# Kernel tuning notes

Measured on AMD Instinct MI355X. Metric: run time of the kernel, lower is better.

The kernel has to match this reference:

```python
import jax, jax.numpy as jnp
import numpy as np

N, E, IN, HID, H, C = 10000, 320000, 64, 64, 4, 64
HC = H * C  # 256


def setup_inputs() -> dict:
    key = jax.random.key(0)
    ks = jax.random.split(key, 40)
    ki = iter(range(40))
    def nrm(shape, scale=0.05):
        return jax.random.normal(ks[next(ki)], shape, dtype=jnp.float32) * scale
    inp = {
        "x": jax.random.normal(ks[next(ki)], (N, IN), dtype=jnp.float32),
        "edge_index": jax.random.randint(ks[next(ki)], (2, E), 0, N, dtype=jnp.int64),
        "lin_w": nrm((IN, HID)), "lin_b": nrm((HID,)),
    }
    dims_in = [HID, HC, HC]
    for i, di in enumerate(dims_in):
        inp[f"gat_w{i}"] = nrm((di, HC))
        inp[f"att_src{i}"] = nrm((H, C))
        inp[f"att_dst{i}"] = nrm((H, C))
        inp[f"gat_b{i}"] = nrm((HC,))
        inp[f"ln_g{i}"] = jnp.ones((HC,), jnp.float32)
        inp[f"ln_b{i}"] = jnp.zeros((HC,), jnp.float32)
    inp["ffn_w1"] = nrm((HC, 2 * HID)); inp["ffn_b1"] = nrm((2 * HID,))
    inp["ffn_w2"] = nrm((2 * HID, 64)); inp["ffn_b2"] = nrm((64,))
    return inp


def _layernorm(x, g, b, eps=1e-5):
    m = jnp.mean(x, -1, keepdims=True)
    v = jnp.var(x, -1, keepdims=True)
    return (x - m) * jax.lax.rsqrt(v + eps) * g + b


def _gat(x, src, dst, w, a_src, a_dst, b):
    # PyG GATConv: per-head linear, additive attention, segment softmax over dst
    xl = (x @ w).reshape(-1, H, C)              # [N,H,C]
    e = jax.nn.leaky_relu(jnp.sum(xl * a_src, -1)[src]
                          + jnp.sum(xl * a_dst, -1)[dst], 0.2)  # [E,H]
    emax = jax.ops.segment_max(e, dst, num_segments=N)
    ex = jnp.exp(e - emax[dst])
    alpha = ex / jax.ops.segment_sum(ex, dst, num_segments=N)[dst]
    out = jax.ops.segment_sum(xl[src] * alpha[:, :, None], dst, num_segments=N)
    return out.reshape(-1, HC) + b


def reference(x, edge_index, lin_w, lin_b,
              gat_w0, att_src0, att_dst0, gat_b0, ln_g0, ln_b0,
              gat_w1, att_src1, att_dst1, gat_b1, ln_g1, ln_b1,
              gat_w2, att_src2, att_dst2, gat_b2, ln_g2, ln_b2,
              ffn_w1, ffn_b1, ffn_w2, ffn_b2):
    loops = jnp.arange(N, dtype=edge_index.dtype)
    src = jnp.concatenate([edge_index[0], loops])  # add_self_loops=True
    dst = jnp.concatenate([edge_index[1], loops])
    h = jax.nn.relu(x @ lin_w + lin_b)
    layers = [(gat_w0, att_src0, att_dst0, gat_b0, ln_g0, ln_b0),
              (gat_w1, att_src1, att_dst1, gat_b1, ln_g1, ln_b1),
              (gat_w2, att_src2, att_dst2, gat_b2, ln_g2, ln_b2)]
    for (w, a_s, a_d, b, g, lb) in layers:
        residual = h
        h = jax.nn.elu(_gat(h, src, dst, w, a_s, a_d, b))
        if residual.shape[-1] != h.shape[-1]:
            residual = jnp.pad(residual, ((0, 0), (0, h.shape[-1] - residual.shape[-1])))
        h = _layernorm(h + residual, g, lb)  # dropout is identity in eval mode
    h = jax.nn.relu(h @ ffn_w1 + ffn_b1)
    return h @ ffn_w2 + ffn_b2
```

## Files before the change

### kernel.cpp

```cpp
#include <hip/hip_runtime.h>

#define N_NODES 10000
#define N_EDGES 320000
#define EL (N_EDGES + N_NODES)
#define HC 256
#define CAP 96

using bf16x8 = __attribute__((ext_vector_type(8))) short;
using f32x4  = __attribute__((ext_vector_type(4))) float;

__device__ __forceinline__ float bf2f(unsigned short u) {
  union { unsigned int i; float f; } v; v.i = ((unsigned int)u) << 16; return v.f;
}
__device__ __forceinline__ unsigned short f2bf(float f) {
  union { float f; unsigned int i; } v; v.f = f;
  unsigned int r = (v.i + 0x7FFFu + ((v.i >> 16) & 1u)) >> 16;
  return (unsigned short)r;
}


__global__ __launch_bounds__(256) void prep_kernel(int* __restrict__ cnt) {
  int i = blockIdx.x * 256 + threadIdx.x;
  if (i < N_NODES) cnt[i] = 0;
}


__device__ __forceinline__ void convw_body(const float* __restrict__ w,
                                           unsigned short* __restrict__ bt,
                                           int K, int idx) {
  int half = K >> 1;
  int col = idx / half;
  int k2 = (idx % half) * 2;
  ushort2 o;
  o.x = f2bf(w[(size_t)k2 * 256 + col]);
  o.y = f2bf(w[(size_t)(k2 + 1) * 256 + col]);
  *(ushort2*)(bt + (size_t)col * K + k2) = o;
}

__global__ __launch_bounds__(256) void scatter_lin_kernel(
    const int* __restrict__ edges, int* __restrict__ cnt, int* __restrict__ slots,
    const float* __restrict__ A, const float* __restrict__ B,
    const float* __restrict__ bias, unsigned short* __restrict__ C,
    const float* __restrict__ w0, unsigned short* __restrict__ bt0,
    const float* __restrict__ w1, unsigned short* __restrict__ bt1,
    const float* __restrict__ w2, unsigned short* __restrict__ bt2) {
  int tid = threadIdx.x;
  int b = blockIdx.x;
  if (b < 1290) {
    int e = b * 256 + tid;
    if (e >= EL) return;
    int s, d;
    if (e < N_EDGES) { s = edges[e]; d = edges[N_EDGES + e]; }
    else { s = d = e - N_EDGES; }
    int pos = atomicAdd(&cnt[d], 1);
    slots[d * CAP + pos] = s;
    return;
  }
  if (b >= 1915) {
    if (b < 1947) convw_body(w0, bt0, 64, (b - 1915) * 256 + tid);
    else if (b < 2075) convw_body(w1, bt1, 256, (b - 1947) * 256 + tid);
    else convw_body(w2, bt2, 256, (b - 2075) * 256 + tid);
    return;
  }
  __shared__ float As[16][36];
  __shared__ float Bs[32][64];
  int row0 = (b - 1290) * 16;
  int g = tid >> 6, lane = tid & 63;
  float acc[4] = {0.f, 0.f, 0.f, 0.f};
  for (int k0 = 0; k0 < 64; k0 += 32) {
    if (tid < 128) {
      int r = tid >> 3;
      int kc = (tid & 7) << 2;
      *(float4*)&As[r][kc] = *(const float4*)(A + (size_t)(row0 + r) * 64 + k0 + kc);
    }
#pragma unroll
    for (int i = 0; i < 2; ++i) {
      int fidx = (i * 256 + tid) * 4;
      *(float4*)&Bs[fidx >> 6][fidx & 63] =
          *(const float4*)(B + (size_t)(k0 + (fidx >> 6)) * 64 + (fidx & 63));
    }
    __syncthreads();
#pragma unroll
    for (int kk = 0; kk < 32; kk += 4) {
      float a4[4][4];
#pragma unroll
      for (int rr = 0; rr < 4; ++rr) {
        float4 t = *(const float4*)&As[g * 4 + rr][kk];
        a4[rr][0] = t.x; a4[rr][1] = t.y; a4[rr][2] = t.z; a4[rr][3] = t.w;
      }
#pragma unroll
      for (int u = 0; u < 4; ++u) {
        float bb = Bs[kk + u][lane];
#pragma unroll
        for (int rr = 0; rr < 4; ++rr) acc[rr] = fmaf(a4[rr][u], bb, acc[rr]);
      }
    }
    __syncthreads();
  }
#pragma unroll
  for (int rr = 0; rr < 4; ++rr) {
    int row = row0 + g * 4 + rr;
    C[(size_t)row * 64 + lane] = f2bf(fmaxf(acc[rr] + bias[lane], 0.f));
  }
}


template <int K>
__global__ __launch_bounds__(256) void gemm_attn_mfma(
    const unsigned short* __restrict__ A, const unsigned short* __restrict__ Bt,
    unsigned short* __restrict__ Cb,
    const float* __restrict__ att_src, const float* __restrict__ att_dst,
    float* __restrict__ asrc_out, float* __restrict__ adst_out) {
  __shared__ __align__(16) unsigned short Asw[16 * 64];
  __shared__ __align__(16) unsigned short Bsw[256 * 64];
  int tid = threadIdx.x;
  int wave = tid >> 6, lane = tid & 63;
  int r = lane & 15, g = lane >> 4;
  int row0 = blockIdx.x * 16;

  f32x4 acc[4];
#pragma unroll
  for (int i = 0; i < 4; ++i) acc[i] = {0.f, 0.f, 0.f, 0.f};

  for (int k0 = 0; k0 < K; k0 += 64) {
    {
      int ar = tid >> 4;
      int kc = (tid & 15) << 2;
      ushort4 av = *(const ushort4*)(A + (size_t)(row0 + ar) * K + k0 + kc);
      *(ushort4*)((char*)Asw + ((ar * 128 + kc * 2) ^ ((ar & 7) << 4))) = av;
    }
#pragma unroll
    for (int i = 0; i < 8; ++i) {
      int idx = i * 256 + tid;
      int col = idx >> 3;
      int kc8 = idx & 7;
      uint4 v = *(const uint4*)(Bt + (size_t)col * K + k0 + kc8 * 8);
      *(uint4*)((char*)Bsw + ((col * 128 + kc8 * 16) ^ ((col & 7) << 4))) = v;
    }
    __syncthreads();
#pragma unroll
    for (int chunk = 0; chunk < 2; ++chunk) {
      bf16x8 af = *(const bf16x8*)((char*)Asw +
                    ((r * 128 + chunk * 64 + g * 16) ^ ((r & 7) << 4)));
#pragma unroll
      for (int i = 0; i < 4; ++i) {
        int col = (wave * 4 + i) * 16 + r;
        bf16x8 bfr = *(const bf16x8*)((char*)Bsw +
                       ((col * 128 + chunk * 64 + g * 16) ^ ((col & 7) << 4)));
        acc[i] = __builtin_amdgcn_mfma_f32_16x16x32_bf16(af, bfr, acc[i], 0, 0, 0);
      }
    }
    __syncthreads();
  }

  float asv[4], adv[4];
#pragma unroll
  for (int i = 0; i < 4; ++i) {
    int col = (wave * 4 + i) * 16 + r;
    asv[i] = att_src[col];
    adv[i] = att_dst[col];
  }
#pragma unroll
  for (int j = 0; j < 4; ++j) {
    float ps = acc[0][j] * asv[0] + acc[1][j] * asv[1] + acc[2][j] * asv[2] + acc[3][j] * asv[3];
    float pd = acc[0][j] * adv[0] + acc[1][j] * adv[1] + acc[2][j] * adv[2] + acc[3][j] * adv[3];
#pragma unroll
    for (int m = 8; m >= 1; m >>= 1) {
      ps += __shfl_xor(ps, m);
      pd += __shfl_xor(pd, m);
    }
    if (r == 0) {
      int row = row0 + g * 4 + j;
      asrc_out[row * 4 + wave] = ps;
      adst_out[row * 4 + wave] = pd;
    }
  }

#pragma unroll
  for (int i = 0; i < 4; ++i) {
    int col = (wave * 4 + i) * 16 + r;
#pragma unroll
    for (int j = 0; j < 4; ++j) {
      int row = row0 + g * 4 + j;
      Cb[(size_t)row * 256 + col] = f2bf(acc[i][j]);
    }
  }
}


template <int MODE>
__global__ __launch_bounds__(256) void agg_kernel(
    const int* __restrict__ cnt, const int* __restrict__ slots,
    const float* __restrict__ asrc, const float* __restrict__ adst,
    const unsigned short* __restrict__ xb, const float* __restrict__ bias,
    const unsigned short* __restrict__ resid, const float* __restrict__ ln_g,
    const float* __restrict__ ln_b, unsigned short* __restrict__ hout) {
  int w = threadIdx.x >> 6, lane = threadIdx.x & 63;
  int n = blockIdx.x * 4 + w;
  int lh = lane & 31;
  int half = lane >> 5;
  int h = lh >> 3;
  int ch8 = lh << 3;
  float ad = adst[n * 4 + h];

  int i0 = n * CAP;
  int deg = cnt[n];
  int len0 = (deg + 1) >> 1;
  int beg = i0 + (half ? len0 : 0);
  int end = i0 + (half ? deg : len0);
  int last = end - 1;

  float a0 = 0.f, a1 = 0.f, a2 = 0.f, a3 = 0.f, a4 = 0.f, a5 = 0.f, a6 = 0.f, a7 = 0.f;
  float wsum = 0.f;

  int sA[4];
#pragma unroll
  for (int j = 0; j < 4; ++j) sA[j] = slots[min(beg + j, last)];
  float ca[4]; uint4 cx[4];
#pragma unroll
  for (int j = 0; j < 4; ++j) {
    ca[j] = asrc[sA[j] * 4 + h];
    cx[j] = *(const uint4*)(xb + (size_t)sA[j] * HC + ch8);
  }
#pragma unroll
  for (int j = 0; j < 4; ++j) sA[j] = slots[min(beg + 4 + j, last)];

  for (int base = beg; base < end; base += 4) {
    float na[4]; uint4 nx[4];
#pragma unroll
    for (int j = 0; j < 4; ++j) {
      na[j] = asrc[sA[j] * 4 + h];
      nx[j] = *(const uint4*)(xb + (size_t)sA[j] * HC + ch8);
    }
#pragma unroll
    for (int j = 0; j < 4; ++j) sA[j] = slots[min(base + 8 + j, last)];
#pragma unroll
    for (int j = 0; j < 4; ++j) {
      float e = ca[j] + ad;
      e = e > 0.f ? e : 0.2f * e;
      float wg = __expf(e);
      wg = (base + j < end) ? wg : 0.f;
      wsum += wg;
      a0 = fmaf(wg, bf2f((unsigned short)(cx[j].x & 0xffff)), a0);
      a1 = fmaf(wg, bf2f((unsigned short)(cx[j].x >> 16)), a1);
      a2 = fmaf(wg, bf2f((unsigned short)(cx[j].y & 0xffff)), a2);
      a3 = fmaf(wg, bf2f((unsigned short)(cx[j].y >> 16)), a3);
      a4 = fmaf(wg, bf2f((unsigned short)(cx[j].z & 0xffff)), a4);
      a5 = fmaf(wg, bf2f((unsigned short)(cx[j].z >> 16)), a5);
      a6 = fmaf(wg, bf2f((unsigned short)(cx[j].w & 0xffff)), a6);
      a7 = fmaf(wg, bf2f((unsigned short)(cx[j].w >> 16)), a7);
    }
#pragma unroll
    for (int j = 0; j < 4; ++j) { ca[j] = na[j]; cx[j] = nx[j]; }
  }

  a0 += __shfl_xor(a0, 32); a1 += __shfl_xor(a1, 32);
  a2 += __shfl_xor(a2, 32); a3 += __shfl_xor(a3, 32);
  a4 += __shfl_xor(a4, 32); a5 += __shfl_xor(a5, 32);
  a6 += __shfl_xor(a6, 32); a7 += __shfl_xor(a7, 32);
  wsum += __shfl_xor(wsum, 32);

  int cb = ch8 + half * 4;
  float v0 = half ? a4 : a0;
  float v1 = half ? a5 : a1;
  float v2 = half ? a6 : a2;
  float v3 = half ? a7 : a3;

  float rw = 1.f / wsum;
  float4 b4 = *(const float4*)(bias + cb);
  v0 = fmaf(v0, rw, b4.x);
  v1 = fmaf(v1, rw, b4.y);
  v2 = fmaf(v2, rw, b4.z);
  v3 = fmaf(v3, rw, b4.w);
  v0 = v0 > 0.f ? v0 : __expf(v0) - 1.f;
  v1 = v1 > 0.f ? v1 : __expf(v1) - 1.f;
  v2 = v2 > 0.f ? v2 : __expf(v2) - 1.f;
  v3 = v3 > 0.f ? v3 : __expf(v3) - 1.f;

  if constexpr (MODE == 0) {
    if (cb < 64) {
      ushort4 r4 = *(const ushort4*)(resid + (size_t)n * 64 + cb);
      v0 += bf2f(r4.x); v1 += bf2f(r4.y); v2 += bf2f(r4.z); v3 += bf2f(r4.w);
    }
  } else {
    ushort4 r4 = *(const ushort4*)(resid + (size_t)n * HC + cb);
    v0 += bf2f(r4.x); v1 += bf2f(r4.y); v2 += bf2f(r4.z); v3 += bf2f(r4.w);
  }

  float s1 = v0 + v1 + v2 + v3;
  float s2 = v0 * v0 + v1 * v1 + v2 * v2 + v3 * v3;
#pragma unroll
  for (int m = 32; m >= 1; m >>= 1) {
    s1 += __shfl_xor(s1, m);
    s2 += __shfl_xor(s2, m);
  }
  float mean = s1 * (1.f / 256.f);
  float var = s2 * (1.f / 256.f) - mean * mean;
  float inv = rsqrtf(var + 1e-5f);

  float4 g4 = *(const float4*)(ln_g + cb);
  float4 lb4 = *(const float4*)(ln_b + cb);
  ushort4 o;
  o.x = f2bf((v0 - mean) * inv * g4.x + lb4.x);
  o.y = f2bf((v1 - mean) * inv * g4.y + lb4.y);
  o.z = f2bf((v2 - mean) * inv * g4.z + lb4.z);
  o.w = f2bf((v3 - mean) * inv * g4.w + lb4.w);
  *(ushort4*)(hout + (size_t)n * HC + cb) = o;
}


__global__ __launch_bounds__(256) void ffn_kernel(const unsigned short* __restrict__ A,
                                                  const float* __restrict__ w1,
                                                  const float* __restrict__ b1,
                                                  const float* __restrict__ w2,
                                                  const float* __restrict__ b2,
                                                  float* __restrict__ out) {
  __shared__ float As[16][36];
  __shared__ float Bs[32][128];
  __shared__ float Ms[16][132];
  int tid = threadIdx.x;
  int row0 = blockIdx.x * 16;
  int g = tid >> 6, lane = tid & 63;

  {
    int colBase = lane * 2;
    float acc[4][2];
#pragma unroll
    for (int r = 0; r < 4; ++r) { acc[r][0] = 0.f; acc[r][1] = 0.f; }
    for (int k0 = 0; k0 < 256; k0 += 32) {
      if (tid < 128) {
        int r = tid >> 3;
        int kc = (tid & 7) << 2;
        ushort4 av = *(const ushort4*)(A + (size_t)(row0 + r) * 256 + k0 + kc);
        As[r][kc]     = bf2f(av.x);
        As[r][kc + 1] = bf2f(av.y);
        As[r][kc + 2] = bf2f(av.z);
        As[r][kc + 3] = bf2f(av.w);
      }
#pragma unroll
      for (int i = 0; i < 4; ++i) {
        int fidx = (i * 256 + tid) * 4;
        *(float4*)&Bs[fidx >> 7][fidx & 127] =
            *(const float4*)(w1 + (size_t)(k0 + (fidx >> 7)) * 128 + (fidx & 127));
      }
      __syncthreads();
#pragma unroll
      for (int kk = 0; kk < 32; kk += 4) {
        float a4[4][4];
#pragma unroll
        for (int rr = 0; rr < 4; ++rr) {
          float4 tv = *(const float4*)&As[g * 4 + rr][kk];
          a4[rr][0] = tv.x; a4[rr][1] = tv.y; a4[rr][2] = tv.z; a4[rr][3] = tv.w;
        }
#pragma unroll
        for (int u = 0; u < 4; ++u) {
          float2 b = *(const float2*)&Bs[kk + u][colBase];
#pragma unroll
          for (int rr = 0; rr < 4; ++rr) {
            acc[rr][0] = fmaf(a4[rr][u], b.x, acc[rr][0]);
            acc[rr][1] = fmaf(a4[rr][u], b.y, acc[rr][1]);
          }
        }
      }
      __syncthreads();
    }
    float bb0 = b1[colBase], bb1 = b1[colBase + 1];
#pragma unroll
    for (int rr = 0; rr < 4; ++rr) {
      Ms[g * 4 + rr][colBase]     = fmaxf(acc[rr][0] + bb0, 0.f);
      Ms[g * 4 + rr][colBase + 1] = fmaxf(acc[rr][1] + bb1, 0.f);
    }
  }
  __syncthreads();

  {
    float acc[4] = {0.f, 0.f, 0.f, 0.f};
    for (int k0 = 0; k0 < 128; k0 += 32) {
#pragma unroll
      for (int i = 0; i < 2; ++i) {
        int fidx = (i * 256 + tid) * 4;
        *(float4*)&Bs[fidx >> 6][fidx & 63] =
            *(const float4*)(w2 + (size_t)(k0 + (fidx >> 6)) * 64 + (fidx & 63));
      }
      __syncthreads();
#pragma unroll
      for (int kk = 0; kk < 32; ++kk) {
        float b = Bs[kk][lane];
#pragma unroll
        for (int rr = 0; rr < 4; ++rr)
          acc[rr] = fmaf(Ms[g * 4 + rr][k0 + kk], b, acc[rr]);
      }
      __syncthreads();
    }
    float bb = b2[lane];
#pragma unroll
    for (int rr = 0; rr < 4; ++rr) {
      int row = row0 + g * 4 + rr;
      out[(size_t)row * 64 + lane] = acc[rr] + bb;
    }
  }
}


extern "C" void kernel_launch(void* const* d_in, const int* in_sizes, int n_in,
                              void* d_out, int out_size, void* d_ws, size_t ws_size,
                              hipStream_t stream) {
  (void)in_sizes; (void)n_in; (void)out_size; (void)ws_size;
  const float* x      = (const float*)d_in[0];
  const int*   edges  = (const int*)d_in[1];
  const float* lin_w  = (const float*)d_in[2];
  const float* lin_b  = (const float*)d_in[3];
  const float* gat_w[3] = {(const float*)d_in[4], (const float*)d_in[10], (const float*)d_in[16]};
  const float* att_s[3] = {(const float*)d_in[5], (const float*)d_in[11], (const float*)d_in[17]};
  const float* att_d[3] = {(const float*)d_in[6], (const float*)d_in[12], (const float*)d_in[18]};
  const float* gat_b[3] = {(const float*)d_in[7], (const float*)d_in[13], (const float*)d_in[19]};
  const float* ln_g[3]  = {(const float*)d_in[8], (const float*)d_in[14], (const float*)d_in[20]};
  const float* ln_b[3]  = {(const float*)d_in[9], (const float*)d_in[15], (const float*)d_in[21]};
  const float* ffn_w1 = (const float*)d_in[22];
  const float* ffn_b1 = (const float*)d_in[23];
  const float* ffn_w2 = (const float*)d_in[24];
  const float* ffn_b2 = (const float*)d_in[25];

  char* p = (char*)d_ws;
  auto alloc = [&](size_t bytes) {
    char* q = p;
    p += (bytes + 255) & ~(size_t)255;
    return q;
  };
  int* cnt   = (int*)alloc(N_NODES * 4);
  int* slots = (int*)alloc((size_t)N_NODES * CAP * 4);
  unsigned short* h0 = (unsigned short*)alloc((size_t)N_NODES * 64 * 2);
  unsigned short* hA = (unsigned short*)alloc((size_t)N_NODES * HC * 2);
  unsigned short* hB = (unsigned short*)alloc((size_t)N_NODES * HC * 2);
  unsigned short* xb = (unsigned short*)alloc((size_t)N_NODES * HC * 2);
  float* as4 = (float*)alloc((size_t)N_NODES * 16);
  float* ad4 = (float*)alloc((size_t)N_NODES * 16);
  unsigned short* bt0 = (unsigned short*)alloc(256 * 64 * 2);
  unsigned short* bt1 = (unsigned short*)alloc(256 * 256 * 2);
  unsigned short* bt2 = (unsigned short*)alloc(256 * 256 * 2);

  const int gblk = N_NODES / 16;
  const int nblk = N_NODES / 4;

  prep_kernel<<<40, 256, 0, stream>>>(cnt);
  scatter_lin_kernel<<<2203, 256, 0, stream>>>(edges, cnt, slots, x, lin_w, lin_b, h0,
                                               gat_w[0], bt0, gat_w[1], bt1, gat_w[2], bt2);

  gemm_attn_mfma<64><<<gblk, 256, 0, stream>>>(h0, bt0, xb, att_s[0], att_d[0], as4, ad4);
  agg_kernel<0><<<nblk, 256, 0, stream>>>(cnt, slots, as4, ad4, xb, gat_b[0], h0,
                                          ln_g[0], ln_b[0], hA);
  gemm_attn_mfma<256><<<gblk, 256, 0, stream>>>(hA, bt1, xb, att_s[1], att_d[1], as4, ad4);
  agg_kernel<1><<<nblk, 256, 0, stream>>>(cnt, slots, as4, ad4, xb, gat_b[1], hA,
                                          ln_g[1], ln_b[1], hB);
  gemm_attn_mfma<256><<<gblk, 256, 0, stream>>>(hB, bt2, xb, att_s[2], att_d[2], as4, ad4);
  agg_kernel<1><<<nblk, 256, 0, stream>>>(cnt, slots, as4, ad4, xb, gat_b[2], hB,
                                          ln_g[2], ln_b[2], hA);

  ffn_kernel<<<gblk, 256, 0, stream>>>(hA, ffn_w1, ffn_b1, ffn_w2, ffn_b2, (float*)d_out);
}
```

Measured before the change: 156.4 us.

## Fuse aggregation with next-layer GEMM and FFN, halving kernel launches

Each GAT aggregation now computes 16 nodes per block, writes the normalized rows into LDS, and immediately runs the next layer's MFMA projection and attention logits from LDS. The last aggregation feeds the FFN directly from LDS. The first linear layer is fused with the layer-0 GEMM, and the weight conversion moves into the prep kernel. Ping-pong buffers are used for xb and the attention scores. This removes kernel launches and global round-trips of the hidden states, but aggregation now runs with only 625 blocks, each wave handling 4 nodes serially, which cuts parallelism and latency hiding.

```diff
diff --git a/kernel.cpp b/kernel.cpp
--- a/kernel.cpp
+++ b/kernel.cpp
@@ -16,12 +16,6 @@
   union { float f; unsigned int i; } v; v.f = f;
   unsigned int r = (v.i + 0x7FFFu + ((v.i >> 16) & 1u)) >> 16;
   return (unsigned short)r;
-}
-
-
-__global__ __launch_bounds__(256) void prep_kernel(int* __restrict__ cnt) {
-  int i = blockIdx.x * 256 + threadIdx.x;
-  if (i < N_NODES) cnt[i] = 0;
 }
 
 
@@ -37,116 +31,58 @@
   *(ushort2*)(bt + (size_t)col * K + k2) = o;
 }
 
-__global__ __launch_bounds__(256) void scatter_lin_kernel(
-    const int* __restrict__ edges, int* __restrict__ cnt, int* __restrict__ slots,
-    const float* __restrict__ A, const float* __restrict__ B,
-    const float* __restrict__ bias, unsigned short* __restrict__ C,
+__global__ __launch_bounds__(256) void prep_kernel(
+    int* __restrict__ cnt,
     const float* __restrict__ w0, unsigned short* __restrict__ bt0,
     const float* __restrict__ w1, unsigned short* __restrict__ bt1,
     const float* __restrict__ w2, unsigned short* __restrict__ bt2) {
-  int tid = threadIdx.x;
-  int b = blockIdx.x;
-  if (b < 1290) {
-    int e = b * 256 + tid;
-    if (e >= EL) return;
-    int s, d;
-    if (e < N_EDGES) { s = edges[e]; d = edges[N_EDGES + e]; }
-    else { s = d = e - N_EDGES; }
-    int pos = atomicAdd(&cnt[d], 1);
-    slots[d * CAP + pos] = s;
-    return;
-  }
-  if (b >= 1915) {
-    if (b < 1947) convw_body(w0, bt0, 64, (b - 1915) * 256 + tid);
-    else if (b < 2075) convw_body(w1, bt1, 256, (b - 1947) * 256 + tid);
-    else convw_body(w2, bt2, 256, (b - 2075) * 256 + tid);
-    return;
-  }
-  __shared__ float As[16][36];
-  __shared__ float Bs[32][64];
-  int row0 = (b - 1290) * 16;
-  int g = tid >> 6, lane = tid & 63;
-  float acc[4] = {0.f, 0.f, 0.f, 0.f};
-  for (int k0 = 0; k0 < 64; k0 += 32) {
-    if (tid < 128) {
-      int r = tid >> 3;
-      int kc = (tid & 7) << 2;
-      *(float4*)&As[r][kc] = *(const float4*)(A + (size_t)(row0 + r) * 64 + k0 + kc);
-    }
-#pragma unroll
-    for (int i = 0; i < 2; ++i) {
-      int fidx = (i * 256 + tid) * 4;
-      *(float4*)&Bs[fidx >> 6][fidx & 63] =
-          *(const float4*)(B + (size_t)(k0 + (fidx >> 6)) * 64 + (fidx & 63));
-    }
-    __syncthreads();
-#pragma unroll
-    for (int kk = 0; kk < 32; kk += 4) {
-      float a4[4][4];
-#pragma unroll
-      for (int rr = 0; rr < 4; ++rr) {
-        float4 t = *(const float4*)&As[g * 4 + rr][kk];
-        a4[rr][0] = t.x; a4[rr][1] = t.y; a4[rr][2] = t.z; a4[rr][3] = t.w;
-      }
-#pragma unroll
-      for (int u = 0; u < 4; ++u) {
-        float bb = Bs[kk + u][lane];
-#pragma unroll
-        for (int rr = 0; rr < 4; ++rr) acc[rr] = fmaf(a4[rr][u], bb, acc[rr]);
-      }
-    }
-    __syncthreads();
-  }
-#pragma unroll
-  for (int rr = 0; rr < 4; ++rr) {
-    int row = row0 + g * 4 + rr;
-    C[(size_t)row * 64 + lane] = f2bf(fmaxf(acc[rr] + bias[lane], 0.f));
+  int b = blockIdx.x, tid = threadIdx.x;
+  if (b < 40) {
+    int i = b * 256 + tid;
+    if (i < N_NODES) cnt[i] = 0;
+  } else if (b < 72) {
+    convw_body(w0, bt0, 64, (b - 40) * 256 + tid);
+  } else if (b < 200) {
+    convw_body(w1, bt1, 256, (b - 72) * 256 + tid);
+  } else {
+    convw_body(w2, bt2, 256, (b - 200) * 256 + tid);
   }
 }
 
 
 template <int K>
-__global__ __launch_bounds__(256) void gemm_attn_mfma(
-    const unsigned short* __restrict__ A, const unsigned short* __restrict__ Bt,
-    unsigned short* __restrict__ Cb,
-    const float* __restrict__ att_src, const float* __restrict__ att_dst,
-    float* __restrict__ asrc_out, float* __restrict__ adst_out) {
-  __shared__ __align__(16) unsigned short Asw[16 * 64];
-  __shared__ __align__(16) unsigned short Bsw[256 * 64];
-  int tid = threadIdx.x;
+__device__ void mfma_from_lds(const char* ALds, char* Bsw,
+                              const unsigned short* __restrict__ Bt,
+                              unsigned short* __restrict__ Cb,
+                              const float* __restrict__ att_src,
+                              const float* __restrict__ att_dst,
+                              float* __restrict__ asrc_out, float* __restrict__ adst_out,
+                              int row0, int tid) {
   int wave = tid >> 6, lane = tid & 63;
   int r = lane & 15, g = lane >> 4;
-  int row0 = blockIdx.x * 16;
 
   f32x4 acc[4];
 #pragma unroll
   for (int i = 0; i < 4; ++i) acc[i] = {0.f, 0.f, 0.f, 0.f};
 
   for (int k0 = 0; k0 < K; k0 += 64) {
-    {
-      int ar = tid >> 4;
-      int kc = (tid & 15) << 2;
-      ushort4 av = *(const ushort4*)(A + (size_t)(row0 + ar) * K + k0 + kc);
-      *(ushort4*)((char*)Asw + ((ar * 128 + kc * 2) ^ ((ar & 7) << 4))) = av;
-    }
 #pragma unroll
     for (int i = 0; i < 8; ++i) {
       int idx = i * 256 + tid;
       int col = idx >> 3;
       int kc8 = idx & 7;
       uint4 v = *(const uint4*)(Bt + (size_t)col * K + k0 + kc8 * 8);
-      *(uint4*)((char*)Bsw + ((col * 128 + kc8 * 16) ^ ((col & 7) << 4))) = v;
+      *(uint4*)(Bsw + ((col * 128 + kc8 * 16) ^ ((col & 7) << 4))) = v;
     }
     __syncthreads();
+    const char* Asl = ALds + (k0 >> 6) * 2048;
 #pragma unroll
     for (int chunk = 0; chunk < 2; ++chunk) {
-      bf16x8 af = *(const bf16x8*)((char*)Asw +
-                    ((r * 128 + chunk * 64 + g * 16) ^ ((r & 7) << 4)));
+      bf16x8 af = *(const bf16x8*)(Asl + ((r * 128 + chunk * 64 + g * 16) ^ ((r & 7) << 4)));
 #pragma unroll
       for (int i = 0; i < 4; ++i) {
         int col = (wave * 4 + i) * 16 + r;
-        bf16x8 bfr = *(const bf16x8*)((char*)Bsw +
-                       ((col * 128 + chunk * 64 + g * 16) ^ ((col & 7) << 4)));
+        bf16x8 bfr = *(const bf16x8*)(Bsw + ((col * 128 + chunk * 64 + g * 16) ^ ((col & 7) << 4)));
         acc[i] = __builtin_amdgcn_mfma_f32_16x16x32_bf16(af, bfr, acc[i], 0, 0, 0);
       }
     }
@@ -189,14 +125,14 @@
 
 
 template <int MODE>
-__global__ __launch_bounds__(256) void agg_kernel(
+__device__ __forceinline__ void agg_node_compute(
+    int n, int lane,
     const int* __restrict__ cnt, const int* __restrict__ slots,
     const float* __restrict__ asrc, const float* __restrict__ adst,
     const unsigned short* __restrict__ xb, const float* __restrict__ bias,
-    const unsigned short* __restrict__ resid, const float* __restrict__ ln_g,
-    const float* __restrict__ ln_b, unsigned short* __restrict__ hout) {
-  int w = threadIdx.x >> 6, lane = threadIdx.x & 63;
-  int n = blockIdx.x * 4 + w;
+    const unsigned short* __restrict__ resid,
+    const float* __restrict__ ln_g, const float* __restrict__ ln_b,
+    float v[4], int& cbOut) {
   int lh = lane & 31;
   int half = lane >> 5;
   int h = lh >> 3;
@@ -300,43 +236,150 @@
 
   float4 g4 = *(const float4*)(ln_g + cb);
   float4 lb4 = *(const float4*)(ln_b + cb);
-  ushort4 o;
-  o.x = f2bf((v0 - mean) * inv * g4.x + lb4.x);
-  o.y = f2bf((v1 - mean) * inv * g4.y + lb4.y);
-  o.z = f2bf((v2 - mean) * inv * g4.z + lb4.z);
-  o.w = f2bf((v3 - mean) * inv * g4.w + lb4.w);
-  *(ushort4*)(hout + (size_t)n * HC + cb) = o;
-}
-
-
-__global__ __launch_bounds__(256) void ffn_kernel(const unsigned short* __restrict__ A,
-                                                  const float* __restrict__ w1,
-                                                  const float* __restrict__ b1,
-                                                  const float* __restrict__ w2,
-                                                  const float* __restrict__ b2,
-                                                  float* __restrict__ out) {
-  __shared__ float As[16][36];
-  __shared__ float Bs[32][128];
-  __shared__ float Ms[16][132];
+  v[0] = (v0 - mean) * inv * g4.x + lb4.x;
+  v[1] = (v1 - mean) * inv * g4.y + lb4.y;
+  v[2] = (v2 - mean) * inv * g4.z + lb4.z;
+  v[3] = (v3 - mean) * inv * g4.w + lb4.w;
+  cbOut = cb;
+}
+
+
+__global__ __launch_bounds__(256) void scatter_linmfma(
+    const int* __restrict__ edges, int* __restrict__ cnt, int* __restrict__ slots,
+    const float* __restrict__ x, const float* __restrict__ lin_w,
+    const float* __restrict__ lin_b, unsigned short* __restrict__ h0,
+    const unsigned short* __restrict__ bt0,
+    const float* __restrict__ as0, const float* __restrict__ ad0,
+    unsigned short* __restrict__ xbA, float* __restrict__ as4A, float* __restrict__ ad4A) {
+  __shared__ __align__(16) char smem[34816];
   int tid = threadIdx.x;
+  int b = blockIdx.x;
+  if (b < 1290) {
+    int e = b * 256 + tid;
+    if (e >= EL) return;
+    int s, d;
+    if (e < N_EDGES) { s = edges[e]; d = edges[N_EDGES + e]; }
+    else { s = d = e - N_EDGES; }
+    int pos = atomicAdd(&cnt[d], 1);
+    slots[d * CAP + pos] = s;
+    return;
+  }
+  int row0 = (b - 1290) * 16;
+  int g = tid >> 6, lane = tid & 63;
+  {
+    float (*As)[36] = (float(*)[36])(smem + 2048);
+    float (*Bs)[64] = (float(*)[64])(smem + 2048 + 2304);
+    float acc[4] = {0.f, 0.f, 0.f, 0.f};
+    for (int k0 = 0; k0 < 64; k0 += 32) {
+      if (tid < 128) {
+        int r = tid >> 3;
+        int kc = (tid & 7) << 2;
+        *(float4*)&As[r][kc] = *(const float4*)(x + (size_t)(row0 + r) * 64 + k0 + kc);
+      }
+#pragma unroll
+      for (int i = 0; i < 2; ++i) {
+        int fidx = (i * 256 + tid) * 4;
+        *(float4*)&Bs[fidx >> 6][fidx & 63] =
+            *(const float4*)(lin_w + (size_t)(k0 + (fidx >> 6)) * 64 + (fidx & 63));
+      }
+      __syncthreads();
+#pragma unroll
+      for (int kk = 0; kk < 32; kk += 4) {
+        float a4[4][4];
+#pragma unroll
+        for (int rr = 0; rr < 4; ++rr) {
+          float4 t = *(const float4*)&As[g * 4 + rr][kk];
+          a4[rr][0] = t.x; a4[rr][1] = t.y; a4[rr][2] = t.z; a4[rr][3] = t.w;
+        }
+#pragma unroll
+        for (int u = 0; u < 4; ++u) {
+          float bb = Bs[kk + u][lane];
+#pragma unroll
+          for (int rr = 0; rr < 4; ++rr) acc[rr] = fmaf(a4[rr][u], bb, acc[rr]);
+        }
+      }
+      __syncthreads();
+    }
+    float bl = lin_b[lane];
+#pragma unroll
+    for (int rr = 0; rr < 4; ++rr) {
+      int r = g * 4 + rr;
+      unsigned short hv = f2bf(fmaxf(acc[rr] + bl, 0.f));
+      h0[(size_t)(row0 + r) * 64 + lane] = hv;
+      *(unsigned short*)(smem + ((r * 128 + lane * 2) ^ ((r & 7) << 4))) = hv;
+    }
+  }
+  __syncthreads();
+  mfma_from_lds<64>(smem, smem + 2048, bt0, xbA, as0, ad0, as4A, ad4A, row0, tid);
+}
+
+
+template <int MODE>
+__global__ __launch_bounds__(256) void aggmfma_kernel(
+    const int* __restrict__ cnt, const int* __restrict__ slots,
+    const float* __restrict__ asrcIn, const float* __restrict__ adstIn,
+    const unsigned short* __restrict__ xbIn, const float* __restrict__ gbias,
+    const unsigned short* __restrict__ resid, const float* __restrict__ ln_g,
+    const float* __restrict__ ln_b, unsigned short* __restrict__ hOut,
+    const unsigned short* __restrict__ Bt, unsigned short* __restrict__ xbOut,
+    const float* __restrict__ att_src, const float* __restrict__ att_dst,
+    float* __restrict__ asrcOut, float* __restrict__ adstOut) {
+  __shared__ __align__(16) char smem[40960];
+  int tid = threadIdx.x;
+  int wave = tid >> 6, lane = tid & 63;
   int row0 = blockIdx.x * 16;
-  int g = tid >> 6, lane = tid & 63;
-
+
+  for (int nl = 0; nl < 4; ++nl) {
+    int r = wave * 4 + nl;
+    int n = row0 + r;
+    float v[4]; int cb;
+    agg_node_compute<MODE>(n, lane, cnt, slots, asrcIn, adstIn, xbIn, gbias,
+                           resid, ln_g, ln_b, v, cb);
+    ushort4 o;
+    o.x = f2bf(v[0]); o.y = f2bf(v[1]); o.z = f2bf(v[2]); o.w = f2bf(v[3]);
+    *(ushort4*)(hOut + (size_t)n * HC + cb) = o;
+    *(ushort4*)(smem + (cb >> 6) * 2048 + ((r * 128 + (cb & 63) * 2) ^ ((r & 7) << 4))) = o;
+  }
+  __syncthreads();
+  mfma_from_lds<256>(smem, smem + 8192, Bt, xbOut, att_src, att_dst,
+                     asrcOut, adstOut, row0, tid);
+}
+
+
+__global__ __launch_bounds__(256) void aggffn_kernel(
+    const int* __restrict__ cnt, const int* __restrict__ slots,
+    const float* __restrict__ asrcIn, const float* __restrict__ adstIn,
+    const unsigned short* __restrict__ xbIn, const float* __restrict__ gbias,
+    const unsigned short* __restrict__ resid, const float* __restrict__ ln_g,
+    const float* __restrict__ ln_b,
+    const float* __restrict__ w1, const float* __restrict__ b1,
+    const float* __restrict__ w2, const float* __restrict__ b2,
+    float* __restrict__ out) {
+  __shared__ __align__(16) char smem[41216];
+  float (*AF)[256] = (float(*)[256])smem;
+  float (*Bs)[128] = (float(*)[128])(smem + 16384);
+  float (*Ms)[132] = (float(*)[132])(smem + 32768);
+  int tid = threadIdx.x;
+  int wave = tid >> 6, lane = tid & 63;
+  int row0 = blockIdx.x * 16;
+
+  for (int nl = 0; nl < 4; ++nl) {
+    int r = wave * 4 + nl;
+    int n = row0 + r;
+    float v[4]; int cb;
+    agg_node_compute<1>(n, lane, cnt, slots, asrcIn, adstIn, xbIn, gbias,
+                        resid, ln_g, ln_b, v, cb);
+    *(float4*)&AF[r][cb] = make_float4(v[0], v[1], v[2], v[3]);
+  }
+  __syncthreads();
+
+  int g = wave;
   {
     int colBase = lane * 2;
     float acc[4][2];
 #pragma unroll
     for (int r = 0; r < 4; ++r) { acc[r][0] = 0.f; acc[r][1] = 0.f; }
     for (int k0 = 0; k0 < 256; k0 += 32) {
-      if (tid < 128) {
-        int r = tid >> 3;
-        int kc = (tid & 7) << 2;
-        ushort4 av = *(const ushort4*)(A + (size_t)(row0 + r) * 256 + k0 + kc);
-        As[r][kc]     = bf2f(av.x);
-        As[r][kc + 1] = bf2f(av.y);
-        As[r][kc + 2] = bf2f(av.z);
-        As[r][kc + 3] = bf2f(av.w);
-      }
 #pragma unroll
       for (int i = 0; i < 4; ++i) {
         int fidx = (i * 256 + tid) * 4;
@@ -349,7 +392,7 @@
         float a4[4][4];
 #pragma unroll
         for (int rr = 0; rr < 4; ++rr) {
-          float4 tv = *(const float4*)&As[g * 4 + rr][kk];
+          float4 tv = *(const float4*)&AF[g * 4 + rr][k0 + kk];
           a4[rr][0] = tv.x; a4[rr][1] = tv.y; a4[rr][2] = tv.z; a4[rr][3] = tv.w;
         }
 #pragma unroll
@@ -432,29 +475,29 @@
   unsigned short* h0 = (unsigned short*)alloc((size_t)N_NODES * 64 * 2);
   unsigned short* hA = (unsigned short*)alloc((size_t)N_NODES * HC * 2);
   unsigned short* hB = (unsigned short*)alloc((size_t)N_NODES * HC * 2);
-  unsigned short* xb = (unsigned short*)alloc((size_t)N_NODES * HC * 2);
-  float* as4 = (float*)alloc((size_t)N_NODES * 16);
-  float* ad4 = (float*)alloc((size_t)N_NODES * 16);
+  unsigned short* xbA = (unsigned short*)alloc((size_t)N_NODES * HC * 2);
+  unsigned short* xbB = (unsigned short*)alloc((size_t)N_NODES * HC * 2);
+  float* as4A = (float*)alloc((size_t)N_NODES * 16);
+  float* ad4A = (float*)alloc((size_t)N_NODES * 16);
+  float* as4B = (float*)alloc((size_t)N_NODES * 16);
+  float* ad4B = (float*)alloc((size_t)N_NODES * 16);
   unsigned short* bt0 = (unsigned short*)alloc(256 * 64 * 2);
   unsigned short* bt1 = (unsigned short*)alloc(256 * 256 * 2);
   unsigned short* bt2 = (unsigned short*)alloc(256 * 256 * 2);
 
   const int gblk = N_NODES / 16;
-  const int nblk = N_NODES / 4;
-
-  prep_kernel<<<40, 256, 0, stream>>>(cnt);
-  scatter_lin_kernel<<<2203, 256, 0, stream>>>(edges, cnt, slots, x, lin_w, lin_b, h0,
-                                               gat_w[0], bt0, gat_w[1], bt1, gat_w[2], bt2);
-
-  gemm_attn_mfma<64><<<gblk, 256, 0, stream>>>(h0, bt0, xb, att_s[0], att_d[0], as4, ad4);
-  agg_kernel<0><<<nblk, 256, 0, stream>>>(cnt, slots, as4, ad4, xb, gat_b[0], h0,
-                                          ln_g[0], ln_b[0], hA);
-  gemm_attn_mfma<256><<<gblk, 256, 0, stream>>>(hA, bt1, xb, att_s[1], att_d[1], as4, ad4);
-  agg_kernel<1><<<nblk, 256, 0, stream>>>(cnt, slots, as4, ad4, xb, gat_b[1], hA,
-                                          ln_g[1], ln_b[1], hB);
-  gemm_attn_mfma<256><<<gblk, 256, 0, stream>>>(hB, bt2, xb, att_s[2], att_d[2], as4, ad4);
-  agg_kernel<1><<<nblk, 256, 0, stream>>>(cnt, slots, as4, ad4, xb, gat_b[2], hB,
-                                          ln_g[2], ln_b[2], hA);
-
-  ffn_kernel<<<gblk, 256, 0, stream>>>(hA, ffn_w1, ffn_b1, ffn_w2, ffn_b2, (float*)d_out);
-}
+
+  prep_kernel<<<328, 256, 0, stream>>>(cnt, gat_w[0], bt0, gat_w[1], bt1, gat_w[2], bt2);
+  scatter_linmfma<<<1290 + gblk, 256, 0, stream>>>(edges, cnt, slots, x, lin_w, lin_b,
+                                                   h0, bt0, att_s[0], att_d[0],
+                                                   xbA, as4A, ad4A);
+  aggmfma_kernel<0><<<gblk, 256, 0, stream>>>(cnt, slots, as4A, ad4A, xbA, gat_b[0],
+                                              h0, ln_g[0], ln_b[0], hA,
+                                              bt1, xbB, att_s[1], att_d[1], as4B, ad4B);
+  aggmfma_kernel<1><<<gblk, 256, 0, stream>>>(cnt, slots, as4B, ad4B, xbB, gat_b[1],
+                                              hA, ln_g[1], ln_b[1], hB,
+                                              bt2, xbA, att_s[2], att_d[2], as4A, ad4A);
+  aggffn_kernel<<<gblk, 256, 0, stream>>>(cnt, slots, as4A, ad4A, xbA, gat_b[2],
+                                          hB, ln_g[2], ln_b[2],
+                                          ffn_w1, ffn_b1, ffn_w2, ffn_b2, (float*)d_out);
+}
```

Result: faster. 151.4 us (median of 2 runs) (-3.2%).
